# Kernel tuning notes

Hardware: AMD Instinct MI355X
Metric: run time of the kernel (lower is better)

Reference implementation:

```python
import jax, jax.numpy as jnp
import numpy as np

HEADS = 8
DIM_HEAD = 64
EPS = 1e-4
SCALE = DIM_HEAD ** -0.5


def setup_inputs() -> dict:
    key = jax.random.key(0)
    k1, k2, k3, k4 = jax.random.split(key, 4)
    dim = HEADS * DIM_HEAD  # 512
    x = jax.random.normal(k1, (2, 2048, dim), dtype=jnp.float32)
    # torch Linear weights are [out, in]; scale like default init
    Wq = jax.random.normal(k2, (dim, dim), dtype=jnp.float32) / np.sqrt(dim)
    Wkv = jax.random.normal(k3, (2 * dim, dim), dtype=jnp.float32) / np.sqrt(dim)
    Wout = jax.random.normal(k4, (dim, dim), dtype=jnp.float32) / np.sqrt(dim)
    return {"x": x, "Wq": Wq, "Wkv": Wkv, "Wout": Wout}


def _normalize_magnitude(t, eps=EPS):
    # divide by (sqrt(mean(t^2, -1)) + eps)
    mag = jnp.sqrt(jnp.mean(t * t, axis=-1, keepdims=True)) + eps
    return t / mag


def reference(x, Wq, Wkv, Wout):
    b, n, dim = x.shape
    h, d = HEADS, DIM_HEAD
    # norm=False -> Identity; context = x (self-attention)
    q = x @ Wq.T                      # [b, n, h*d]
    kv = x @ Wkv.T                    # [b, n, 2*h*d]
    k, v = jnp.split(kv, 2, axis=-1)
    def to_heads(t):
        return t.reshape(b, n, h, d).transpose(0, 2, 1, 3)  # [b, h, n, d]
    q, k, v = map(to_heads, (q, k, v))
    q = _normalize_magnitude(q)
    k = _normalize_magnitude(k)
    sim = jnp.einsum('bhid,bhjd->bhij', q, k) * SCALE
    attn = jax.nn.softmax(sim, axis=-1)
    out = jnp.einsum('bhij,bhjd->bhid', attn, v)
    out = out.transpose(0, 2, 1, 3).reshape(b, n, h * d)
    return out @ Wout.T
```

## Files before the change

### kernel.cpp

```cpp
#include <hip/hip_runtime.h>

typedef __bf16 bf16x8 __attribute__((ext_vector_type(8)));
typedef __bf16 bf16x4 __attribute__((ext_vector_type(4)));
typedef float  f32x4  __attribute__((ext_vector_type(4)));

#define LOG2E_F 1.44269504088896340736f

static constexpr int kB = 2, kN = 2048, kH = 8, kD = 64, kDim = 512;
static constexpr int kTok = kB * kN;
static constexpr int kNQKV = 1536;
static constexpr int kKH = 3;

__device__ __forceinline__ void gld16(const void* g, void* l) {
  __builtin_amdgcn_global_load_lds(
      (const __attribute__((address_space(1))) void*)g,
      (__attribute__((address_space(3))) void*)l, 16, 0, 0);
}


__global__ __launch_bounds__(256) void cvt_all(const float* __restrict__ x,
                                               const float* __restrict__ wq,
                                               const float* __restrict__ wkv,
                                               const float* __restrict__ wo,
                                               __bf16* __restrict__ xb,
                                               __bf16* __restrict__ wqkvb,
                                               __bf16* __restrict__ wob) {
  size_t i = ((size_t)blockIdx.x * 256 + threadIdx.x) * 8;
  const float* s; __bf16* d; size_t off;
  if (i < 2097152)      { s = x;   d = xb;              off = i; }
  else if (i < 2359296) { s = wq;  d = wqkvb;           off = i - 2097152; }
  else if (i < 2883584) { s = wkv; d = wqkvb + 262144;  off = i - 2359296; }
  else                  { s = wo;  d = wob;             off = i - 2883584; }
  float4 u = *(const float4*)(s + off);
  float4 v = *(const float4*)(s + off + 4);
  bf16x8 t;
  t[0] = (__bf16)u.x; t[1] = (__bf16)u.y; t[2] = (__bf16)u.z; t[3] = (__bf16)u.w;
  t[4] = (__bf16)v.x; t[5] = (__bf16)v.y; t[6] = (__bf16)v.z; t[7] = (__bf16)v.w;
  *(bf16x8*)(d + off) = t;
}

__global__ __launch_bounds__(256, 3) void gemm_qkv(const __bf16* __restrict__ A,
                                                   const __bf16* __restrict__ B,
                                                   __bf16* __restrict__ qn,
                                                   __bf16* __restrict__ kn,
                                                   __bf16* __restrict__ vt2) {
  const int K = kDim;
  const int tid = threadIdx.x;
  const int w = tid >> 6, lane = tid & 63, quad = lane >> 4, lq = lane & 15;
  const int m0 = blockIdx.y * 128;
  const int n0 = blockIdx.x * 64;
  const int wm = w * 32;
  __shared__ __bf16 As[2][128 * 64];
  __shared__ __bf16 Bs[2][64 * 64];

  const f32x4 zero = {0.f, 0.f, 0.f, 0.f};
  f32x4 acc[2][4];
#pragma unroll
  for (int fm = 0; fm < 2; ++fm)
#pragma unroll
    for (int fn = 0; fn < 4; ++fn) acc[fm][fn] = zero;

  const int sr = tid >> 3, ch = tid & 7;
  auto stage = [&](int k0, int buf) {
#pragma unroll
    for (int j = 0; j < 4; ++j) {
      const int row = j * 32 + sr;
      gld16(A + (size_t)(m0 + row) * K + k0 + ((ch ^ (row & 7)) << 3),
            &As[buf][row * 64 + ch * 8]);
    }
#pragma unroll
    for (int j = 0; j < 2; ++j) {
      const int row = j * 32 + sr;
      gld16(B + (size_t)(n0 + row) * K + k0 + ((ch ^ (row & 7)) << 3),
            &Bs[buf][row * 64 + ch * 8]);
    }
  };
  const int sw0 = ((quad ^ (lq & 7)) << 3);
  const int sw1 = (((4 | quad) ^ (lq & 7)) << 3);

  stage(0, 0);
  for (int i = 0; i < 8; ++i) {
    __syncthreads();
    if (i + 1 < 8) stage((i + 1) << 6, (i + 1) & 1);
    const __bf16* as = As[i & 1];
    const __bf16* bs = Bs[i & 1];
#pragma unroll
    for (int ks = 0; ks < 2; ++ks) {
      const int sw = ks ? sw1 : sw0;
      bf16x8 a[2], b[4];
#pragma unroll
      for (int fm = 0; fm < 2; ++fm)
        a[fm] = *(const bf16x8*)&as[(wm + fm * 16 + lq) * 64 + sw];
#pragma unroll
      for (int fn = 0; fn < 4; ++fn)
        b[fn] = *(const bf16x8*)&bs[(fn * 16 + lq) * 64 + sw];
#pragma unroll
      for (int fm = 0; fm < 2; ++fm)
#pragma unroll
        for (int fn = 0; fn < 4; ++fn)
          acc[fm][fn] =
              __builtin_amdgcn_mfma_f32_16x16x32_bf16(a[fm], b[fn], acc[fm][fn], 0, 0, 0);
    }
  }

  const int h = (n0 >> 6) & 7;
  if (n0 >= 1024) {
    __syncthreads();
    __bf16* Ts = &As[0][0];
#pragma unroll
    for (int fm = 0; fm < 2; ++fm)
#pragma unroll
      for (int r = 0; r < 4; ++r) {
        const int mo = wm + fm * 16 + quad * 4 + r;
        const int tau = mo >> 6, tt = mo & 63;
        const int p = (tt & 15) * 4 + (tt >> 4);
#pragma unroll
        for (int fn = 0; fn < 4; ++fn)
          Ts[tau * 4608 + (fn * 16 + lq) * 72 + p] = (__bf16)acc[fm][fn][r];
      }
    __syncthreads();
    const int b = m0 >> 11, kt0 = (m0 & (kN - 1)) >> 6;
    const int dd = tid >> 2, p0 = (tid & 3) << 4;
#pragma unroll
    for (int tau = 0; tau < 2; ++tau) {
      const __bf16* src = Ts + tau * 4608 + dd * 72 + p0;
      __bf16* dst = vt2 + ((size_t)((b * kH + h) * 32 + kt0 + tau)) * 4096 + tid * 16;
      *(bf16x8*)dst = *(const bf16x8*)src;
      *(bf16x8*)(dst + 8) = *(const bf16x8*)(src + 8);
    }
  } else {
    const float qs = (n0 < 512) ? (0.125f * LOG2E_F) : 1.0f;
    __bf16* dst0 = (n0 < 512) ? qn : kn;
#pragma unroll
    for (int fm = 0; fm < 2; ++fm)
#pragma unroll
      for (int r = 0; r < 4; ++r) {
        float ss = 0.f;
#pragma unroll
        for (int fn = 0; fn < 4; ++fn) ss += acc[fm][fn][r] * acc[fm][fn][r];
#pragma unroll
        for (int off = 1; off < 16; off <<= 1) ss += __shfl_xor(ss, off, 64);
        const float inv = qs / (sqrtf(ss * (1.f / 64)) + 1e-4f);
        const int m = m0 + wm + fm * 16 + quad * 4 + r;
        const int b = m >> 11, n = m & (kN - 1);
        __bf16* dst = dst0 + ((size_t)(b * kH + h) * kN + n) * kD;
#pragma unroll
        for (int fn = 0; fn < 4; ++fn)
          dst[fn * 16 + lq] = (__bf16)(acc[fm][fn][r] * inv);
      }
  }
}

__global__ __launch_bounds__(256, 3) void attn(const __bf16* __restrict__ qn,
                                               const __bf16* __restrict__ kn,
                                               const __bf16* __restrict__ vt2,
                                               __bf16* __restrict__ po,
                                               float* __restrict__ pl) {
  const int qt = blockIdx.x, bh = blockIdx.y, kh = blockIdx.z;
  const int kt0 = kh * 11;
  const int cnt = (kh == 2) ? 10 : 11;
  const int tid = threadIdx.x;
  const int w = tid >> 6, lane = tid & 63, quad = lane >> 4, lq = lane & 15;
  __shared__ __bf16 Ks[2][4096];
  __shared__ __bf16 Vs[2][4096];
  __shared__ __bf16 Ps[4][32 * 72];
  __bf16* myP = Ps[w];

  bf16x8 aq[2][2];
#pragma unroll
  for (int fm = 0; fm < 2; ++fm) {
    const __bf16* Qb = qn + ((size_t)bh * kN + qt * 128 + w * 32 + fm * 16 + lq) * kD;
    aq[fm][0] = *(const bf16x8*)(Qb + quad * 8);
    aq[fm][1] = *(const bf16x8*)(Qb + 32 + quad * 8);
  }

  const f32x4 zero  = {0.f, 0.f, 0.f, 0.f};
  const f32x4 minit = {-12.f, -12.f, -12.f, -12.f};
  f32x4 o[2][4];
  float lr[2][4];
#pragma unroll
  for (int fm = 0; fm < 2; ++fm)
#pragma unroll
    for (int i = 0; i < 4; ++i) { o[fm][i] = zero; lr[fm][i] = 0.f; }

  const __bf16* Kb = kn + (size_t)bh * kN * kD;
  const __bf16* Vb = vt2 + (size_t)bh * 32 * 4096;

  auto stage = [&](int ktg, int buf) {
#pragma unroll
    for (int j = 0; j < 2; ++j) {
      const int s = j * 256 + tid;
      const int row = s >> 3, ch = s & 7;
      const int src = row * 64 + ((ch ^ (row & 7)) << 3);
      gld16(Kb + (size_t)ktg * 4096 + src, &Ks[buf][s * 8]);
      gld16(Vb + (size_t)ktg * 4096 + src, &Vs[buf][s * 8]);
    }
  };
  const int sw0 = ((quad ^ (lq & 7)) << 3);
  const int sw1 = (((4 | quad) ^ (lq & 7)) << 3);

  stage(kt0, 0);
  for (int kt = 0; kt < cnt; ++kt) {
    __syncthreads();
    if (kt + 1 < cnt) stage(kt0 + kt + 1, (kt + 1) & 1);
    const __bf16* ks_ = Ks[kt & 1];
    const __bf16* vs_ = Vs[kt & 1];

    bf16x8 kb0[4], kb1[4], vb0[4], vb1[4];
#pragma unroll
    for (int fn = 0; fn < 4; ++fn) {
      const int rb = (fn * 16 + lq) * 64;
      kb0[fn] = *(const bf16x8*)&ks_[rb + sw0];
      kb1[fn] = *(const bf16x8*)&ks_[rb + sw1];
      vb0[fn] = *(const bf16x8*)&vs_[rb + sw0];
      vb1[fn] = *(const bf16x8*)&vs_[rb + sw1];
    }
    f32x4 s[2][4];
#pragma unroll
    for (int fm = 0; fm < 2; ++fm)
#pragma unroll
      for (int fn = 0; fn < 4; ++fn) {
        f32x4 a = __builtin_amdgcn_mfma_f32_16x16x32_bf16(aq[fm][0], kb0[fn], minit, 0, 0, 0);
        s[fm][fn] = __builtin_amdgcn_mfma_f32_16x16x32_bf16(aq[fm][1], kb1[fn], a, 0, 0, 0);
      }

#pragma unroll
    for (int fm = 0; fm < 2; ++fm)
#pragma unroll
      for (int r = 0; r < 4; ++r) {
        const float p0 = __builtin_amdgcn_exp2f(s[fm][0][r]);
        const float p1 = __builtin_amdgcn_exp2f(s[fm][1][r]);
        const float p2 = __builtin_amdgcn_exp2f(s[fm][2][r]);
        const float p3 = __builtin_amdgcn_exp2f(s[fm][3][r]);
        lr[fm][r] += (p0 + p1) + (p2 + p3);
        bf16x4 pk = {(__bf16)p0, (__bf16)p1, (__bf16)p2, (__bf16)p3};
        *(bf16x4*)&myP[(fm * 16 + quad * 4 + r) * 72 + lq * 4] = pk;
      }

#pragma unroll
    for (int fm = 0; fm < 2; ++fm) {
      bf16x8 ap0 = *(const bf16x8*)&myP[(fm * 16 + lq) * 72 + quad * 8];
      bf16x8 ap1 = *(const bf16x8*)&myP[(fm * 16 + lq) * 72 + 32 + quad * 8];
#pragma unroll
      for (int fn = 0; fn < 4; ++fn) {
        o[fm][fn] = __builtin_amdgcn_mfma_f32_16x16x32_bf16(ap0, vb0[fn], o[fm][fn], 0, 0, 0);
        o[fm][fn] = __builtin_amdgcn_mfma_f32_16x16x32_bf16(ap1, vb1[fn], o[fm][fn], 0, 0, 0);
      }
    }
  }

  const int b = bh >> 3, h = bh & 7;
#pragma unroll
  for (int fm = 0; fm < 2; ++fm) {
    const int qrow0 = qt * 128 + w * 32 + fm * 16 + quad * 4;
#pragma unroll
    for (int r = 0; r < 4; ++r) {
      float sum = lr[fm][r];
#pragma unroll
      for (int off = 1; off < 16; off <<= 1) sum += __shfl_xor(sum, off, 64);
      if (lq == 0) pl[(size_t)kh * 32768 + bh * kN + qrow0 + r] = sum;
      const size_t ob = ((size_t)kh * kTok + b * kN + qrow0 + r) * kDim + h * 64;
#pragma unroll
      for (int fn = 0; fn < 4; ++fn) po[ob + fn * 16 + lq] = (__bf16)o[fm][fn][r];
    }
  }
}

__global__ __launch_bounds__(256) void combine(const __bf16* __restrict__ po,
                                               const float* __restrict__ pl,
                                               __bf16* __restrict__ ao) {
  const size_t i = ((size_t)blockIdx.x * 256 + threadIdx.x) * 4;
  const int tok = (int)(i >> 9), dk = (int)(i & 511);
  const int h = dk >> 6, b = tok >> 11, qrow = tok & (kN - 1);
  const int idx = (b * kH + h) * kN + qrow;
  float l = 0.f;
#pragma unroll
  for (int kh = 0; kh < kKH; ++kh) l += pl[kh * 32768 + idx];
  const float inv = 1.f / l;
  float s0 = 0.f, s1 = 0.f, s2 = 0.f, s3 = 0.f;
#pragma unroll
  for (int kh = 0; kh < kKH; ++kh) {
    bf16x4 a = *(const bf16x4*)(po + (size_t)kh * kTok * kDim + i);
    s0 += (float)a[0]; s1 += (float)a[1]; s2 += (float)a[2]; s3 += (float)a[3];
  }
  bf16x4 t = {(__bf16)(s0 * inv), (__bf16)(s1 * inv),
              (__bf16)(s2 * inv), (__bf16)(s3 * inv)};
  *(bf16x4*)(ao + i) = t;
}

__global__ __launch_bounds__(256, 2) void gemm64(const __bf16* __restrict__ A,
                                                 const __bf16* __restrict__ B,
                                                 float* __restrict__ C,
                                                 int N, int K) {
  const int tid = threadIdx.x;
  const int w = tid >> 6, lane = tid & 63, quad = lane >> 4, lq = lane & 15;
  const int m0 = blockIdx.y * 64;
  const int n0 = blockIdx.x * 64;
  const int wm = (w >> 1) * 32, wn = (w & 1) * 32;
  __shared__ __bf16 As[2][4096];
  __shared__ __bf16 Bs[2][4096];

  const f32x4 zero = {0.f, 0.f, 0.f, 0.f};
  f32x4 acc00 = zero, acc01 = zero, acc10 = zero, acc11 = zero;

  const int sr = tid >> 3, ch = tid & 7;
  auto stage = [&](int k0, int buf) {
#pragma unroll
    for (int j = 0; j < 2; ++j) {
      const int row = j * 32 + sr;
      const int src = k0 + ((ch ^ (row & 7)) << 3);
      gld16(A + (size_t)(m0 + row) * K + src, &As[buf][row * 64 + ch * 8]);
      gld16(B + (size_t)(n0 + row) * K + src, &Bs[buf][row * 64 + ch * 8]);
    }
  };
  const int sw0 = ((quad ^ (lq & 7)) << 3);
  const int sw1 = (((4 | quad) ^ (lq & 7)) << 3);

  stage(0, 0);
  const int iters = K >> 6;
  for (int i = 0; i < iters; ++i) {
    __syncthreads();
    if (i + 1 < iters) stage((i + 1) << 6, (i + 1) & 1);
    const __bf16* as = As[i & 1];
    const __bf16* bs = Bs[i & 1];
#pragma unroll
    for (int ks = 0; ks < 2; ++ks) {
      const int sw = ks ? sw1 : sw0;
      bf16x8 a0 = *(const bf16x8*)&as[(wm +      lq) * 64 + sw];
      bf16x8 a1 = *(const bf16x8*)&as[(wm + 16 + lq) * 64 + sw];
      bf16x8 b0 = *(const bf16x8*)&bs[(wn +      lq) * 64 + sw];
      bf16x8 b1 = *(const bf16x8*)&bs[(wn + 16 + lq) * 64 + sw];
      acc00 = __builtin_amdgcn_mfma_f32_16x16x32_bf16(a0, b0, acc00, 0, 0, 0);
      acc01 = __builtin_amdgcn_mfma_f32_16x16x32_bf16(a0, b1, acc01, 0, 0, 0);
      acc10 = __builtin_amdgcn_mfma_f32_16x16x32_bf16(a1, b0, acc10, 0, 0, 0);
      acc11 = __builtin_amdgcn_mfma_f32_16x16x32_bf16(a1, b1, acc11, 0, 0, 0);
    }
  }
  const f32x4 av[2][2] = {{acc00, acc01}, {acc10, acc11}};
#pragma unroll
  for (int fm = 0; fm < 2; ++fm)
#pragma unroll
    for (int fn = 0; fn < 2; ++fn)
#pragma unroll
      for (int r = 0; r < 4; ++r)
        C[(size_t)(m0 + wm + fm * 16 + quad * 4 + r) * N + (n0 + wn + fn * 16 + lq)] =
            av[fm][fn][r];
}

extern "C" void kernel_launch(void* const* d_in, const int* in_sizes, int n_in,
                              void* d_out, int out_size, void* d_ws, size_t ws_size,
                              hipStream_t stream) {
  const float* x    = (const float*)d_in[0];
  const float* Wq   = (const float*)d_in[1];
  const float* Wkv  = (const float*)d_in[2];
  const float* Wout = (const float*)d_in[3];
  float* out = (float*)d_out;
  char* ws = (char*)d_ws;

  __bf16* xb    = (__bf16*)(ws);
  __bf16* wqkvb = (__bf16*)(ws + (size_t)(4 << 20));
  __bf16* wob   = (__bf16*)(ws + (size_t)(6 << 20));
  __bf16* qn    = (__bf16*)(ws + (size_t)(7 << 20));
  __bf16* kn    = (__bf16*)(ws + (size_t)(11 << 20));
  __bf16* vt2   = (__bf16*)(ws + (size_t)(15 << 20));
  __bf16* po    = (__bf16*)(ws + (size_t)(19 << 20));
  float*  pl    = (float*)(ws + (size_t)(32 << 20));
  __bf16* ao    = (__bf16*)(ws + (size_t)(33 << 20));

  cvt_all<<<1536, 256, 0, stream>>>(x, Wq, Wkv, Wout, xb, wqkvb, wob);
  gemm_qkv<<<dim3(kNQKV / 64, kTok / 128), 256, 0, stream>>>(xb, wqkvb, qn, kn, vt2);
  attn<<<dim3(kN / 128, kB * kH, kKH), 256, 0, stream>>>(qn, kn, vt2, po, pl);
  combine<<<kTok * kDim / 1024, 256, 0, stream>>>(po, pl, ao);
  gemm64<<<dim3(kDim / 64, kTok / 64), 256, 0, stream>>>(ao, wob, out, kDim, kDim);
}
```

Before: 118.2 us.

## Replace split-KV attention plus combine with single-pass 64-row query tiles

The attention kernel no longer splits the key range into three chunks with a separate combine kernel. Each block now handles 64 query rows (16 per wave) over all 32 key tiles and normalizes by the row sum directly into the output buffer, removing the partial-output writes, the combine launch and its extra memory traffic. The grid becomes 512 blocks with a swizzled mapping of block index to (query tile, head). The trade-off is less K/V reuse per block, since each staged tile now feeds only 16 query rows per wave, and longer serial loops per block.

```diff
diff --git a/kernel.cpp b/kernel.cpp
--- a/kernel.cpp
+++ b/kernel.cpp
@@ -9,7 +9,6 @@
 static constexpr int kB = 2, kN = 2048, kH = 8, kD = 64, kDim = 512;
 static constexpr int kTok = kB * kN;
 static constexpr int kNQKV = 1536;
-static constexpr int kKH = 3;
 
 __device__ __forceinline__ void gld16(const void* g, void* l) {
   __builtin_amdgcn_global_load_lds(
@@ -154,34 +153,27 @@
 __global__ __launch_bounds__(256, 3) void attn(const __bf16* __restrict__ qn,
                                                const __bf16* __restrict__ kn,
                                                const __bf16* __restrict__ vt2,
-                                               __bf16* __restrict__ po,
-                                               float* __restrict__ pl) {
-  const int qt = blockIdx.x, bh = blockIdx.y, kh = blockIdx.z;
-  const int kt0 = kh * 11;
-  const int cnt = (kh == 2) ? 10 : 11;
+                                               __bf16* __restrict__ ao) {
+  const int bid = blockIdx.x;
+  const int swz = (bid & 7) * 64 + (bid >> 3);
+  const int qt = swz & 31, bh = swz >> 5;
   const int tid = threadIdx.x;
   const int w = tid >> 6, lane = tid & 63, quad = lane >> 4, lq = lane & 15;
   __shared__ __bf16 Ks[2][4096];
   __shared__ __bf16 Vs[2][4096];
-  __shared__ __bf16 Ps[4][32 * 72];
+  __shared__ __bf16 Ps[4][16 * 72];
   __bf16* myP = Ps[w];
 
-  bf16x8 aq[2][2];
-#pragma unroll
-  for (int fm = 0; fm < 2; ++fm) {
-    const __bf16* Qb = qn + ((size_t)bh * kN + qt * 128 + w * 32 + fm * 16 + lq) * kD;
-    aq[fm][0] = *(const bf16x8*)(Qb + quad * 8);
-    aq[fm][1] = *(const bf16x8*)(Qb + 32 + quad * 8);
-  }
+  const __bf16* Qb = qn + ((size_t)bh * kN + qt * 64 + w * 16 + lq) * kD;
+  const bf16x8 aq0 = *(const bf16x8*)(Qb + quad * 8);
+  const bf16x8 aq1 = *(const bf16x8*)(Qb + 32 + quad * 8);
 
   const f32x4 zero  = {0.f, 0.f, 0.f, 0.f};
   const f32x4 minit = {-12.f, -12.f, -12.f, -12.f};
-  f32x4 o[2][4];
-  float lr[2][4];
-#pragma unroll
-  for (int fm = 0; fm < 2; ++fm)
-#pragma unroll
-    for (int i = 0; i < 4; ++i) { o[fm][i] = zero; lr[fm][i] = 0.f; }
+  f32x4 o[4];
+  float lr[4];
+#pragma unroll
+  for (int i = 0; i < 4; ++i) { o[i] = zero; lr[i] = 0.f; }
 
   const __bf16* Kb = kn + (size_t)bh * kN * kD;
   const __bf16* Vb = vt2 + (size_t)bh * 32 * 4096;
@@ -199,10 +191,10 @@
   const int sw0 = ((quad ^ (lq & 7)) << 3);
   const int sw1 = (((4 | quad) ^ (lq & 7)) << 3);
 
-  stage(kt0, 0);
-  for (int kt = 0; kt < cnt; ++kt) {
-    __syncthreads();
-    if (kt + 1 < cnt) stage(kt0 + kt + 1, (kt + 1) & 1);
+  stage(0, 0);
+  for (int kt = 0; kt < 32; ++kt) {
+    __syncthreads();
+    if (kt + 1 < 32) stage(kt + 1, (kt + 1) & 1);
     const __bf16* ks_ = Ks[kt & 1];
     const __bf16* vs_ = Vs[kt & 1];
 
@@ -215,77 +207,45 @@
       vb0[fn] = *(const bf16x8*)&vs_[rb + sw0];
       vb1[fn] = *(const bf16x8*)&vs_[rb + sw1];
     }
-    f32x4 s[2][4];
-#pragma unroll
-    for (int fm = 0; fm < 2; ++fm)
-#pragma unroll
-      for (int fn = 0; fn < 4; ++fn) {
-        f32x4 a = __builtin_amdgcn_mfma_f32_16x16x32_bf16(aq[fm][0], kb0[fn], minit, 0, 0, 0);
-        s[fm][fn] = __builtin_amdgcn_mfma_f32_16x16x32_bf16(aq[fm][1], kb1[fn], a, 0, 0, 0);
-      }
-
-#pragma unroll
-    for (int fm = 0; fm < 2; ++fm)
-#pragma unroll
-      for (int r = 0; r < 4; ++r) {
-        const float p0 = __builtin_amdgcn_exp2f(s[fm][0][r]);
-        const float p1 = __builtin_amdgcn_exp2f(s[fm][1][r]);
-        const float p2 = __builtin_amdgcn_exp2f(s[fm][2][r]);
-        const float p3 = __builtin_amdgcn_exp2f(s[fm][3][r]);
-        lr[fm][r] += (p0 + p1) + (p2 + p3);
-        bf16x4 pk = {(__bf16)p0, (__bf16)p1, (__bf16)p2, (__bf16)p3};
-        *(bf16x4*)&myP[(fm * 16 + quad * 4 + r) * 72 + lq * 4] = pk;
-      }
-
-#pragma unroll
-    for (int fm = 0; fm < 2; ++fm) {
-      bf16x8 ap0 = *(const bf16x8*)&myP[(fm * 16 + lq) * 72 + quad * 8];
-      bf16x8 ap1 = *(const bf16x8*)&myP[(fm * 16 + lq) * 72 + 32 + quad * 8];
-#pragma unroll
-      for (int fn = 0; fn < 4; ++fn) {
-        o[fm][fn] = __builtin_amdgcn_mfma_f32_16x16x32_bf16(ap0, vb0[fn], o[fm][fn], 0, 0, 0);
-        o[fm][fn] = __builtin_amdgcn_mfma_f32_16x16x32_bf16(ap1, vb1[fn], o[fm][fn], 0, 0, 0);
-      }
+    f32x4 s[4];
+#pragma unroll
+    for (int fn = 0; fn < 4; ++fn) {
+      f32x4 a = __builtin_amdgcn_mfma_f32_16x16x32_bf16(aq0, kb0[fn], minit, 0, 0, 0);
+      s[fn] = __builtin_amdgcn_mfma_f32_16x16x32_bf16(aq1, kb1[fn], a, 0, 0, 0);
+    }
+
+#pragma unroll
+    for (int r = 0; r < 4; ++r) {
+      const float p0 = __builtin_amdgcn_exp2f(s[0][r]);
+      const float p1 = __builtin_amdgcn_exp2f(s[1][r]);
+      const float p2 = __builtin_amdgcn_exp2f(s[2][r]);
+      const float p3 = __builtin_amdgcn_exp2f(s[3][r]);
+      lr[r] += (p0 + p1) + (p2 + p3);
+      bf16x4 pk = {(__bf16)p0, (__bf16)p1, (__bf16)p2, (__bf16)p3};
+      *(bf16x4*)&myP[(quad * 4 + r) * 72 + lq * 4] = pk;
+    }
+
+    const bf16x8 ap0 = *(const bf16x8*)&myP[lq * 72 + quad * 8];
+    const bf16x8 ap1 = *(const bf16x8*)&myP[lq * 72 + 32 + quad * 8];
+#pragma unroll
+    for (int fn = 0; fn < 4; ++fn) {
+      o[fn] = __builtin_amdgcn_mfma_f32_16x16x32_bf16(ap0, vb0[fn], o[fn], 0, 0, 0);
+      o[fn] = __builtin_amdgcn_mfma_f32_16x16x32_bf16(ap1, vb1[fn], o[fn], 0, 0, 0);
     }
   }
 
   const int b = bh >> 3, h = bh & 7;
 #pragma unroll
-  for (int fm = 0; fm < 2; ++fm) {
-    const int qrow0 = qt * 128 + w * 32 + fm * 16 + quad * 4;
-#pragma unroll
-    for (int r = 0; r < 4; ++r) {
-      float sum = lr[fm][r];
-#pragma unroll
-      for (int off = 1; off < 16; off <<= 1) sum += __shfl_xor(sum, off, 64);
-      if (lq == 0) pl[(size_t)kh * 32768 + bh * kN + qrow0 + r] = sum;
-      const size_t ob = ((size_t)kh * kTok + b * kN + qrow0 + r) * kDim + h * 64;
-#pragma unroll
-      for (int fn = 0; fn < 4; ++fn) po[ob + fn * 16 + lq] = (__bf16)o[fm][fn][r];
-    }
-  }
-}
-
-__global__ __launch_bounds__(256) void combine(const __bf16* __restrict__ po,
-                                               const float* __restrict__ pl,
-                                               __bf16* __restrict__ ao) {
-  const size_t i = ((size_t)blockIdx.x * 256 + threadIdx.x) * 4;
-  const int tok = (int)(i >> 9), dk = (int)(i & 511);
-  const int h = dk >> 6, b = tok >> 11, qrow = tok & (kN - 1);
-  const int idx = (b * kH + h) * kN + qrow;
-  float l = 0.f;
-#pragma unroll
-  for (int kh = 0; kh < kKH; ++kh) l += pl[kh * 32768 + idx];
-  const float inv = 1.f / l;
-  float s0 = 0.f, s1 = 0.f, s2 = 0.f, s3 = 0.f;
-#pragma unroll
-  for (int kh = 0; kh < kKH; ++kh) {
-    bf16x4 a = *(const bf16x4*)(po + (size_t)kh * kTok * kDim + i);
-    s0 += (float)a[0]; s1 += (float)a[1]; s2 += (float)a[2]; s3 += (float)a[3];
-  }
-  bf16x4 t = {(__bf16)(s0 * inv), (__bf16)(s1 * inv),
-              (__bf16)(s2 * inv), (__bf16)(s3 * inv)};
-  *(bf16x4*)(ao + i) = t;
+  for (int r = 0; r < 4; ++r) {
+    float sum = lr[r];
+#pragma unroll
+    for (int off = 1; off < 16; off <<= 1) sum += __shfl_xor(sum, off, 64);
+    const float inv = 1.f / sum;
+    const int row = qt * 64 + w * 16 + quad * 4 + r;
+    __bf16* dst = ao + ((size_t)(b * kN + row)) * kDim + h * 64;
+#pragma unroll
+    for (int fn = 0; fn < 4; ++fn) dst[fn * 16 + lq] = (__bf16)(o[fn][r] * inv);
+  }
 }
 
 __global__ __launch_bounds__(256, 2) void gemm64(const __bf16* __restrict__ A,
@@ -363,13 +323,10 @@
   __bf16* qn    = (__bf16*)(ws + (size_t)(7 << 20));
   __bf16* kn    = (__bf16*)(ws + (size_t)(11 << 20));
   __bf16* vt2   = (__bf16*)(ws + (size_t)(15 << 20));
-  __bf16* po    = (__bf16*)(ws + (size_t)(19 << 20));
-  float*  pl    = (float*)(ws + (size_t)(32 << 20));
-  __bf16* ao    = (__bf16*)(ws + (size_t)(33 << 20));
+  __bf16* ao    = (__bf16*)(ws + (size_t)(19 << 20));
 
   cvt_all<<<1536, 256, 0, stream>>>(x, Wq, Wkv, Wout, xb, wqkvb, wob);
   gemm_qkv<<<dim3(kNQKV / 64, kTok / 128), 256, 0, stream>>>(xb, wqkvb, qn, kn, vt2);
-  attn<<<dim3(kN / 128, kB * kH, kKH), 256, 0, stream>>>(qn, kn, vt2, po, pl);
-  combine<<<kTok * kDim / 1024, 256, 0, stream>>>(po, pl, ao);
+  attn<<<kN / 64 * kB * kH, 256, 0, stream>>>(qn, kn, vt2, ao);
   gemm64<<<dim3(kDim / 64, kTok / 64), 256, 0, stream>>>(ao, wob, out, kDim, kDim);
 }
```

New measurement: 121.0 us. 1.02x slower.

## Drop split-K attention and combine kernel; use 64-row query tiles with 2 waves

Applied to the files above, without the earlier changes.

Replaces the 3-way split over key tiles, with its partial output buffers and separate combine kernel, by a single pass over all 32 key tiles per block. The block is now 128 threads covering 64 query rows, which gives 512 blocks, and a swizzled 1D block index spreads heads across the grid. Each block normalizes its own output, removing one launch and the partial write/read traffic. In exchange, each block now walks a longer serial loop and every K/V tile is staged once per 64 query rows instead of once per 128, which doubles K/V loads.

```diff
diff --git a/kernel.cpp b/kernel.cpp
--- a/kernel.cpp
+++ b/kernel.cpp
@@ -9,7 +9,6 @@
 static constexpr int kB = 2, kN = 2048, kH = 8, kD = 64, kDim = 512;
 static constexpr int kTok = kB * kN;
 static constexpr int kNQKV = 1536;
-static constexpr int kKH = 3;
 
 __device__ __forceinline__ void gld16(const void* g, void* l) {
   __builtin_amdgcn_global_load_lds(
@@ -151,25 +150,24 @@
   }
 }
 
-__global__ __launch_bounds__(256, 3) void attn(const __bf16* __restrict__ qn,
+__global__ __launch_bounds__(128, 2) void attn(const __bf16* __restrict__ qn,
                                                const __bf16* __restrict__ kn,
                                                const __bf16* __restrict__ vt2,
-                                               __bf16* __restrict__ po,
-                                               float* __restrict__ pl) {
-  const int qt = blockIdx.x, bh = blockIdx.y, kh = blockIdx.z;
-  const int kt0 = kh * 11;
-  const int cnt = (kh == 2) ? 10 : 11;
+                                               __bf16* __restrict__ ao) {
+  const int bid = blockIdx.x;
+  const int swz = (bid & 7) * 64 + (bid >> 3);
+  const int qt = swz & 31, bh = swz >> 5;
   const int tid = threadIdx.x;
   const int w = tid >> 6, lane = tid & 63, quad = lane >> 4, lq = lane & 15;
   __shared__ __bf16 Ks[2][4096];
   __shared__ __bf16 Vs[2][4096];
-  __shared__ __bf16 Ps[4][32 * 72];
+  __shared__ __bf16 Ps[2][32 * 72];
   __bf16* myP = Ps[w];
 
   bf16x8 aq[2][2];
 #pragma unroll
   for (int fm = 0; fm < 2; ++fm) {
-    const __bf16* Qb = qn + ((size_t)bh * kN + qt * 128 + w * 32 + fm * 16 + lq) * kD;
+    const __bf16* Qb = qn + ((size_t)bh * kN + qt * 64 + w * 32 + fm * 16 + lq) * kD;
     aq[fm][0] = *(const bf16x8*)(Qb + quad * 8);
     aq[fm][1] = *(const bf16x8*)(Qb + 32 + quad * 8);
   }
@@ -188,8 +186,8 @@
 
   auto stage = [&](int ktg, int buf) {
 #pragma unroll
-    for (int j = 0; j < 2; ++j) {
-      const int s = j * 256 + tid;
+    for (int j = 0; j < 4; ++j) {
+      const int s = j * 128 + tid;
       const int row = s >> 3, ch = s & 7;
       const int src = row * 64 + ((ch ^ (row & 7)) << 3);
       gld16(Kb + (size_t)ktg * 4096 + src, &Ks[buf][s * 8]);
@@ -199,10 +197,10 @@
   const int sw0 = ((quad ^ (lq & 7)) << 3);
   const int sw1 = (((4 | quad) ^ (lq & 7)) << 3);
 
-  stage(kt0, 0);
-  for (int kt = 0; kt < cnt; ++kt) {
-    __syncthreads();
-    if (kt + 1 < cnt) stage(kt0 + kt + 1, (kt + 1) & 1);
+  stage(0, 0);
+  for (int kt = 0; kt < 32; ++kt) {
+    __syncthreads();
+    if (kt + 1 < 32) stage(kt + 1, (kt + 1) & 1);
     const __bf16* ks_ = Ks[kt & 1];
     const __bf16* vs_ = Vs[kt & 1];
 
@@ -239,8 +237,8 @@
 
 #pragma unroll
     for (int fm = 0; fm < 2; ++fm) {
-      bf16x8 ap0 = *(const bf16x8*)&myP[(fm * 16 + lq) * 72 + quad * 8];
-      bf16x8 ap1 = *(const bf16x8*)&myP[(fm * 16 + lq) * 72 + 32 + quad * 8];
+      const bf16x8 ap0 = *(const bf16x8*)&myP[(fm * 16 + lq) * 72 + quad * 8];
+      const bf16x8 ap1 = *(const bf16x8*)&myP[(fm * 16 + lq) * 72 + 32 + quad * 8];
 #pragma unroll
       for (int fn = 0; fn < 4; ++fn) {
         o[fm][fn] = __builtin_amdgcn_mfma_f32_16x16x32_bf16(ap0, vb0[fn], o[fm][fn], 0, 0, 0);
@@ -251,41 +249,18 @@
 
   const int b = bh >> 3, h = bh & 7;
 #pragma unroll
-  for (int fm = 0; fm < 2; ++fm) {
-    const int qrow0 = qt * 128 + w * 32 + fm * 16 + quad * 4;
+  for (int fm = 0; fm < 2; ++fm)
 #pragma unroll
     for (int r = 0; r < 4; ++r) {
       float sum = lr[fm][r];
 #pragma unroll
       for (int off = 1; off < 16; off <<= 1) sum += __shfl_xor(sum, off, 64);
-      if (lq == 0) pl[(size_t)kh * 32768 + bh * kN + qrow0 + r] = sum;
-      const size_t ob = ((size_t)kh * kTok + b * kN + qrow0 + r) * kDim + h * 64;
-#pragma unroll
-      for (int fn = 0; fn < 4; ++fn) po[ob + fn * 16 + lq] = (__bf16)o[fm][fn][r];
-    }
-  }
-}
-
-__global__ __launch_bounds__(256) void combine(const __bf16* __restrict__ po,
-                                               const float* __restrict__ pl,
-                                               __bf16* __restrict__ ao) {
-  const size_t i = ((size_t)blockIdx.x * 256 + threadIdx.x) * 4;
-  const int tok = (int)(i >> 9), dk = (int)(i & 511);
-  const int h = dk >> 6, b = tok >> 11, qrow = tok & (kN - 1);
-  const int idx = (b * kH + h) * kN + qrow;
-  float l = 0.f;
-#pragma unroll
-  for (int kh = 0; kh < kKH; ++kh) l += pl[kh * 32768 + idx];
-  const float inv = 1.f / l;
-  float s0 = 0.f, s1 = 0.f, s2 = 0.f, s3 = 0.f;
-#pragma unroll
-  for (int kh = 0; kh < kKH; ++kh) {
-    bf16x4 a = *(const bf16x4*)(po + (size_t)kh * kTok * kDim + i);
-    s0 += (float)a[0]; s1 += (float)a[1]; s2 += (float)a[2]; s3 += (float)a[3];
-  }
-  bf16x4 t = {(__bf16)(s0 * inv), (__bf16)(s1 * inv),
-              (__bf16)(s2 * inv), (__bf16)(s3 * inv)};
-  *(bf16x4*)(ao + i) = t;
+      const float inv = 1.f / sum;
+      const int row = qt * 64 + w * 32 + fm * 16 + quad * 4 + r;
+      __bf16* dst = ao + ((size_t)(b * kN + row)) * kDim + h * 64;
+#pragma unroll
+      for (int fn = 0; fn < 4; ++fn) dst[fn * 16 + lq] = (__bf16)(o[fm][fn][r] * inv);
+    }
 }
 
 __global__ __launch_bounds__(256, 2) void gemm64(const __bf16* __restrict__ A,
@@ -363,13 +338,10 @@
   __bf16* qn    = (__bf16*)(ws + (size_t)(7 << 20));
   __bf16* kn    = (__bf16*)(ws + (size_t)(11 << 20));
   __bf16* vt2   = (__bf16*)(ws + (size_t)(15 << 20));
-  __bf16* po    = (__bf16*)(ws + (size_t)(19 << 20));
-  float*  pl    = (float*)(ws + (size_t)(32 << 20));
-  __bf16* ao    = (__bf16*)(ws + (size_t)(33 << 20));
+  __bf16* ao    = (__bf16*)(ws + (size_t)(19 << 20));
 
   cvt_all<<<1536, 256, 0, stream>>>(x, Wq, Wkv, Wout, xb, wqkvb, wob);
   gemm_qkv<<<dim3(kNQKV / 64, kTok / 128), 256, 0, stream>>>(xb, wqkvb, qn, kn, vt2);
-  attn<<<dim3(kN / 128, kB * kH, kKH), 256, 0, stream>>>(qn, kn, vt2, po, pl);
-  combine<<<kTok * kDim / 1024, 256, 0, stream>>>(po, pl, ao);
+  attn<<<kN / 64 * kB * kH, 128, 0, stream>>>(qn, kn, vt2, ao);
   gemm64<<<dim3(kDim / 64, kTok / 64), 256, 0, stream>>>(ao, wob, out, kDim, kDim);
 }
```

New measurement: 129.4 us. 1.09x slower.

## Fuse split-K attention combine into output projection GEMM and add MFMA priority hints

Applied to the files above, without the earlier changes.

Removes the separate combine kernel. The output-projection GEMM now reads the three split-KV partial outputs and row sums itself, normalizes them, and writes the bf16 A tile into LDS. This saves one launch and a full round trip of the combined activation through global memory. The cost is that each N-block reloads and recombines the same partial data eight times, and A staging becomes synchronous register loads instead of async global-to-LDS copies. It also raises wave priority around the MFMA sections of the attention loop.

```diff
diff --git a/kernel.cpp b/kernel.cpp
--- a/kernel.cpp
+++ b/kernel.cpp
@@ -216,6 +216,7 @@
       vb1[fn] = *(const bf16x8*)&vs_[rb + sw1];
     }
     f32x4 s[2][4];
+    __builtin_amdgcn_s_setprio(1);
 #pragma unroll
     for (int fm = 0; fm < 2; ++fm)
 #pragma unroll
@@ -223,6 +224,7 @@
         f32x4 a = __builtin_amdgcn_mfma_f32_16x16x32_bf16(aq[fm][0], kb0[fn], minit, 0, 0, 0);
         s[fm][fn] = __builtin_amdgcn_mfma_f32_16x16x32_bf16(aq[fm][1], kb1[fn], a, 0, 0, 0);
       }
+    __builtin_amdgcn_s_setprio(0);
 
 #pragma unroll
     for (int fm = 0; fm < 2; ++fm)
@@ -237,6 +239,7 @@
         *(bf16x4*)&myP[(fm * 16 + quad * 4 + r) * 72 + lq * 4] = pk;
       }
 
+    __builtin_amdgcn_s_setprio(1);
 #pragma unroll
     for (int fm = 0; fm < 2; ++fm) {
       bf16x8 ap0 = *(const bf16x8*)&myP[(fm * 16 + lq) * 72 + quad * 8];
@@ -247,6 +250,7 @@
         o[fm][fn] = __builtin_amdgcn_mfma_f32_16x16x32_bf16(ap1, vb1[fn], o[fm][fn], 0, 0, 0);
       }
     }
+    __builtin_amdgcn_s_setprio(0);
   }
 
   const int b = bh >> 3, h = bh & 7;
@@ -266,32 +270,11 @@
   }
 }
 
-__global__ __launch_bounds__(256) void combine(const __bf16* __restrict__ po,
-                                               const float* __restrict__ pl,
-                                               __bf16* __restrict__ ao) {
-  const size_t i = ((size_t)blockIdx.x * 256 + threadIdx.x) * 4;
-  const int tok = (int)(i >> 9), dk = (int)(i & 511);
-  const int h = dk >> 6, b = tok >> 11, qrow = tok & (kN - 1);
-  const int idx = (b * kH + h) * kN + qrow;
-  float l = 0.f;
-#pragma unroll
-  for (int kh = 0; kh < kKH; ++kh) l += pl[kh * 32768 + idx];
-  const float inv = 1.f / l;
-  float s0 = 0.f, s1 = 0.f, s2 = 0.f, s3 = 0.f;
-#pragma unroll
-  for (int kh = 0; kh < kKH; ++kh) {
-    bf16x4 a = *(const bf16x4*)(po + (size_t)kh * kTok * kDim + i);
-    s0 += (float)a[0]; s1 += (float)a[1]; s2 += (float)a[2]; s3 += (float)a[3];
-  }
-  bf16x4 t = {(__bf16)(s0 * inv), (__bf16)(s1 * inv),
-              (__bf16)(s2 * inv), (__bf16)(s3 * inv)};
-  *(bf16x4*)(ao + i) = t;
-}
-
-__global__ __launch_bounds__(256, 2) void gemm64(const __bf16* __restrict__ A,
-                                                 const __bf16* __restrict__ B,
-                                                 float* __restrict__ C,
-                                                 int N, int K) {
+__global__ __launch_bounds__(256, 2) void gemm64c(const __bf16* __restrict__ po,
+                                                  const float* __restrict__ pl,
+                                                  const __bf16* __restrict__ B,
+                                                  float* __restrict__ C) {
+  const int N = kDim, K = kDim;
   const int tid = threadIdx.x;
   const int w = tid >> 6, lane = tid & 63, quad = lane >> 4, lq = lane & 15;
   const int m0 = blockIdx.y * 64;
@@ -304,23 +287,44 @@
   f32x4 acc00 = zero, acc01 = zero, acc10 = zero, acc11 = zero;
 
   const int sr = tid >> 3, ch = tid & 7;
-  auto stage = [&](int k0, int buf) {
+  auto stageA = [&](int k0, int buf) {
+    const int h = k0 >> 6;
+#pragma unroll
+    for (int j = 0; j < 2; ++j) {
+      const int row = j * 32 + sr;
+      const int m = m0 + row;
+      const int b = m >> 11, qrow = m & (kN - 1);
+      const int idx = ((b * kH + h) << 11) + qrow;
+      const float l = pl[idx] + pl[32768 + idx] + pl[65536 + idx];
+      const float inv = 1.f / l;
+      const size_t off = (size_t)m * K + k0 + ch * 8;
+      const bf16x8 p0 = *(const bf16x8*)(po + off);
+      const bf16x8 p1 = *(const bf16x8*)(po + (size_t)kTok * kDim + off);
+      const bf16x8 p2 = *(const bf16x8*)(po + 2 * (size_t)kTok * kDim + off);
+      bf16x8 t;
+#pragma unroll
+      for (int e = 0; e < 8; ++e)
+        t[e] = (__bf16)((((float)p0[e] + (float)p1[e]) + (float)p2[e]) * inv);
+      *(bf16x8*)&As[buf][row * 64 + ((ch ^ (row & 7)) << 3)] = t;
+    }
+  };
+  auto stageB = [&](int k0, int buf) {
 #pragma unroll
     for (int j = 0; j < 2; ++j) {
       const int row = j * 32 + sr;
       const int src = k0 + ((ch ^ (row & 7)) << 3);
-      gld16(A + (size_t)(m0 + row) * K + src, &As[buf][row * 64 + ch * 8]);
       gld16(B + (size_t)(n0 + row) * K + src, &Bs[buf][row * 64 + ch * 8]);
     }
   };
   const int sw0 = ((quad ^ (lq & 7)) << 3);
   const int sw1 = (((4 | quad) ^ (lq & 7)) << 3);
 
-  stage(0, 0);
+  stageA(0, 0);
+  stageB(0, 0);
   const int iters = K >> 6;
   for (int i = 0; i < iters; ++i) {
     __syncthreads();
-    if (i + 1 < iters) stage((i + 1) << 6, (i + 1) & 1);
+    if (i + 1 < iters) { stageA((i + 1) << 6, (i + 1) & 1); stageB((i + 1) << 6, (i + 1) & 1); }
     const __bf16* as = As[i & 1];
     const __bf16* bs = Bs[i & 1];
 #pragma unroll
@@ -365,11 +369,9 @@
   __bf16* vt2   = (__bf16*)(ws + (size_t)(15 << 20));
   __bf16* po    = (__bf16*)(ws + (size_t)(19 << 20));
   float*  pl    = (float*)(ws + (size_t)(32 << 20));
-  __bf16* ao    = (__bf16*)(ws + (size_t)(33 << 20));
 
   cvt_all<<<1536, 256, 0, stream>>>(x, Wq, Wkv, Wout, xb, wqkvb, wob);
   gemm_qkv<<<dim3(kNQKV / 64, kTok / 128), 256, 0, stream>>>(xb, wqkvb, qn, kn, vt2);
   attn<<<dim3(kN / 128, kB * kH, kKH), 256, 0, stream>>>(qn, kn, vt2, po, pl);
-  combine<<<kTok * kDim / 1024, 256, 0, stream>>>(po, pl, ao);
-  gemm64<<<dim3(kDim / 64, kTok / 64), 256, 0, stream>>>(ao, wob, out, kDim, kDim);
-}
+  gemm64c<<<dim3(kDim / 64, kTok / 64), 256, 0, stream>>>(po, pl, wob, out);
+}
```

Result: slower. 122.4 us (+3.6%).
